# Performance work log

Measured on AMD Instinct MI355X. Metric: run time of the kernel, lower is better.

## Reference

```python
import jax, jax.numpy as jnp
import numpy as np

GROUP = 32          # microscale group size for both acts and weights
FP8_MAX = 448.0     # float8_e4m3fn max
FP4_TABLE = jnp.array([0.0, 0.5, 1.0, 1.5, 2.0, 3.0, 4.0, 6.0,
                       -0.0, -0.5, -1.0, -1.5, -2.0, -3.0, -4.0, -6.0], dtype=jnp.float32)


def _ue8m0_to_float(sf):
    # uint8 exponent byte placed directly into the fp32 exponent field: 2^(e-127)
    return jax.lax.bitcast_convert_type(sf.astype(jnp.uint32) << 23, jnp.float32)


def _dequant_mxfp4(w_packed, sf):
    # w_packed: [..., K//2] ints in [0,256), two e2m1 nibbles per byte (low nibble = even elem)
    lo = FP4_TABLE[w_packed & 0xF]
    hi = FP4_TABLE[(w_packed >> 4) & 0xF]
    w = jnp.stack([lo, hi], axis=-1).reshape(*w_packed.shape[:-1], -1)   # [..., K]
    s = _ue8m0_to_float(sf)                                              # [..., K//32]
    w = w.reshape(*sf.shape, GROUP) * s[..., None]
    return w.reshape(*w_packed.shape[:-1], 2 * w_packed.shape[-1])


def _quant_dequant_fp8(x):
    # Faithful to _deepseek_v4_stage_mega_moe_inputs_kernel: per-32-group amax,
    # scale = amax/448 rounded UP to a power of two (UE8M0), cast to fp8 e4m3.
    T, D = x.shape
    xg = x.reshape(T, D // GROUP, GROUP)
    amax = jnp.maximum(jnp.max(jnp.abs(xg), axis=-1), 1e-4)
    scale = amax / FP8_MAX
    bits = jax.lax.bitcast_convert_type(scale, jnp.uint32)
    exp = ((bits >> 23) & 0xFF) + ((bits & 0x7FFFFF) != 0).astype(jnp.uint32)
    exp = jnp.clip(exp, 1, 254)
    rscale = jax.lax.bitcast_convert_type(exp << 23, jnp.float32)
    q = (xg * (1.0 / rscale)[..., None]).astype(jnp.float8_e4m3fn)
    return (q.astype(jnp.float32) * rscale[..., None]).reshape(T, D)


def setup_inputs() -> dict:
    key = jax.random.key(0)
    ks = jax.random.split(key, 7)
    T, D, I, E, K = 512, 2048, 768, 16, 8
    hidden_states = jax.random.normal(ks[0], (T, D), dtype=jnp.float32)
    topk_weights = jax.random.uniform(ks[1], (T, K), dtype=jnp.float32)
    topk_weights = topk_weights / jnp.sum(topk_weights, axis=-1, keepdims=True)
    topk_ids = jax.random.randint(ks[2], (T, K), 0, E, dtype=jnp.int32)
    w13_weight = jax.random.randint(ks[3], (E, 2 * I, D // 2), 0, 256, dtype=jnp.int32)
    w13_weight_scale = jax.random.randint(ks[4], (E, 2 * I, D // GROUP), 120, 128, dtype=jnp.int32)
    w2_weight = jax.random.randint(ks[5], (E, D, I // 2), 0, 256, dtype=jnp.int32)
    w2_weight_scale = jax.random.randint(ks[6], (E, D, I // GROUP), 120, 128, dtype=jnp.int32)
    return {"hidden_states": hidden_states, "topk_weights": topk_weights,
            "topk_ids": topk_ids, "w13_weight": w13_weight,
            "w13_weight_scale": w13_weight_scale, "w2_weight": w2_weight,
            "w2_weight_scale": w2_weight_scale}


def reference(hidden_states, topk_weights, topk_ids, w13_weight, w13_weight_scale,
              w2_weight, w2_weight_scale):
    E = w13_weight.shape[0]
    I = w13_weight.shape[1] // 2
    x = _quant_dequant_fp8(hidden_states)                 # [T, D] fp8-quantized acts
    w13 = _dequant_mxfp4(w13_weight, w13_weight_scale)    # [E, 2I, D]
    w2 = _dequant_mxfp4(w2_weight, w2_weight_scale)       # [E, D, I]
    onehot = (topk_ids[:, :, None] == jnp.arange(E)[None, None, :]).astype(jnp.float32)  # [T,K,E]
    routed = jnp.any(onehot > 0, axis=1)                  # [T, E]
    Xe = routed.T[:, :, None].astype(x.dtype) * x[None]   # [E, T, D]
    h = jnp.einsum('etd,efd->etf', Xe, w13)               # [E, T, 2I]
    gate, up = h[..., :I], h[..., I:]
    a = jax.nn.silu(gate) * up                            # SiluAndMul
    ye = jnp.einsum('eti,edi->etd', a, w2)                # [E, T, D]
    comb = jnp.einsum('tke,tk->te', onehot, topk_weights) # [T, E] routing weights
    return jnp.einsum('te,etd->td', comb, ye)             # [T, D]
```

## Files before the change

### kernel.cpp

```cpp
#include <hip/hip_runtime.h>
#include <stdint.h>
#include <math.h>

#define T_TOK 512
#define DDIM  2048
#define IDIM  768
#define NEXP  16
#define TOPK  8
#define LDB   72

typedef __attribute__((ext_vector_type(8))) short bf16x8;
typedef __attribute__((ext_vector_type(4))) float f32x4;

__device__ __forceinline__ float e4m3_rtne(float f) {
  uint32_t u = __float_as_uint(f);
  uint32_t sign = u & 0x80000000u;
  uint32_t a = u & 0x7FFFFFFFu;
  float fa = __uint_as_float(a);
  float out;
  if (fa >= 0.015625f) {
    uint32_t lsb = (a >> 20) & 1u;
    a += 0x0007FFFFu + lsb;
    a &= 0xFFF00000u;
    out = __uint_as_float(a);
  } else {
    out = rintf(fa * 512.0f) * 0.001953125f;
  }
  return __uint_as_float(__float_as_uint(out) | sign);
}

__global__ void qdq_kernel(const float* __restrict__ x, ushort* __restrict__ xq) {
  int idx = blockIdx.x * 256 + threadIdx.x;
  float v = x[idx];
  float a = fabsf(v);
#pragma unroll
  for (int m = 16; m >= 1; m >>= 1)
    a = fmaxf(a, __shfl_xor(a, m, 32));
  a = fmaxf(a, 1e-4f);
  float scale = a / 448.0f;
  uint32_t b = __float_as_uint(scale);
  uint32_t ex = ((b >> 23) & 255u) + ((b & 0x7FFFFFu) ? 1u : 0u);
  ex = ex < 1u ? 1u : (ex > 254u ? 254u : ex);
  float rscale = __uint_as_float(ex << 23);
  float inv = 1.0f / rscale;
  float r = e4m3_rtne(v * inv) * rscale;
  xq[idx] = (ushort)(__float_as_uint(r) >> 16);
}

__global__ void route_kernel(const int* __restrict__ ids, const float* __restrict__ wts,
                             int* counts, int* offsets, int* lists, float* combs,
                             int* tpe, int* tps, int* tpn) {
  int t = threadIdx.x;
  int  myid[TOPK];
  float myw[TOPK];
#pragma unroll
  for (int k = 0; k < TOPK; k++) { myid[k] = ids[t*TOPK+k]; myw[k] = wts[t*TOPK+k]; }
  int np = 0;
  for (int e = 0; e < NEXP; e++) {
    float s = 0.f; bool r = false;
#pragma unroll
    for (int k = 0; k < TOPK; k++) if (myid[k] == e) { s += myw[k]; r = true; }
    if (r) {
      int slot = atomicAdd(&counts[e], 1);
      lists[(e<<9) + slot] = t;
      combs[(e<<9) + slot] = s;
      tpe[t*TOPK + np] = e;
      tps[t*TOPK + np] = slot;
      np++;
    }
  }
  tpn[t] = np;
  __syncthreads();
  if (t == 0) {
    int acc = 0;
    for (int e = 0; e < NEXP; e++) {
      offsets[e] = acc;
      acc += atomicAdd(&counts[e], 0);
    }
    offsets[NEXP] = acc;
  }
}

__device__ __forceinline__ uint32_t dec2(uint32_t w8, uint32_t S) {
  uint32_t lo = w8 & 15u, hi = (w8 >> 4) & 15u;
  uint32_t mlo = lo & 7u, mhi = hi & 7u;
  uint32_t clo = (mlo < 2u) ? 0u : mlo;
  uint32_t chi = (mhi < 2u) ? 0u : mhi;
  uint32_t blo = (mlo == 0u) ? 0u : ((S + clo) << 6);
  uint32_t bhi = (mhi == 0u) ? 0u : ((S + chi) << 6);
  blo |= (lo & 8u) << 12;
  bhi |= (hi & 8u) << 12;
  return blo | (bhi << 16);
}

__global__ __launch_bounds__(256,3) void gemm1_kernel(
    const ushort* __restrict__ xq, const int* __restrict__ w13,
    const int* __restrict__ w13s, const int* __restrict__ counts,
    const int* __restrict__ offsets, const int* __restrict__ lists,
    const float* __restrict__ combs, ushort* __restrict__ a_buf)
{
  const int e  = blockIdx.x;
  const int i0 = blockIdx.y << 5;
  const int m0 = blockIdx.z << 7;
  const int cnt = counts[e];
  if (m0 >= cnt) return;

  __shared__ __align__(16) ushort Bsh[2][64*LDB];
  __shared__ int   toks[128];
  __shared__ float cmbs[128];

  const int tid = threadIdx.x;
  if (tid < 128) {
    int m = m0 + tid; bool v = m < cnt;
    toks[tid] = v ? lists[(e<<9)+m] : 0;
    cmbs[tid] = v ? combs[(e<<9)+m] : 0.f;
  }
  __syncthreads();

  const int wv = tid >> 6, l = tid & 63, l16 = l & 15, q = l >> 4;

  const ushort* arow[2];
#pragma unroll
  for (int i = 0; i < 2; i++)
    arow[i] = xq + (size_t)toks[wv*32 + i*16 + l16]*DDIM + q*8;

  const int rb = tid >> 2, hq = tid & 3;
  const int feat = (rb < 32) ? (i0 + rb) : (IDIM + i0 + (rb - 32));
  const int* wrow = w13 + ((size_t)e*(2*IDIM) + feat)*(DDIM/2) + hq*8;
  const int* srow = w13s + ((size_t)e*(2*IDIM) + feat)*(DDIM/32) + (hq >> 1);
  const int bdst = rb*LDB + hq*16;

  f32x4 acc[2][4];
#pragma unroll
  for (int i = 0; i < 2; i++)
#pragma unroll
    for (int j = 0; j < 4; j++) acc[i][j] = (f32x4){0.f,0.f,0.f,0.f};

  bf16x8 afr[2][2];
#pragma unroll
  for (int i = 0; i < 2; i++)
#pragma unroll
    for (int s = 0; s < 2; s++)
      afr[i][s] = *(const bf16x8*)(arow[i] + s*32);
  {
    int4 w0 = *(const int4*)(wrow);
    int4 w1 = *(const int4*)(wrow + 4);
    uint32_t S = (((uint32_t)srow[0]) - 1u) << 1;
    int wi[8] = {w0.x,w0.y,w0.z,w0.w, w1.x,w1.y,w1.z,w1.w};
    uint32_t od[8];
#pragma unroll
    for (int c = 0; c < 8; c++) od[c] = dec2((uint32_t)wi[c], S);
    ushort* d = &Bsh[0][bdst];
    *(uint4*)d       = make_uint4(od[0], od[1], od[2], od[3]);
    *(uint4*)(d + 8) = make_uint4(od[4], od[5], od[6], od[7]);
  }
  __syncthreads();

  for (int k0 = 0; k0 < DDIM; k0 += 64) {
    const int cur = (k0 >> 6) & 1;
    const bool more = (k0 + 64) < DDIM;

    int4 nw0, nw1; uint32_t nS = 0;
    bf16x8 nafr[2][2];
    if (more) {
      const int* wp = wrow + ((k0 + 64) >> 1);
      nw0 = *(const int4*)wp;
      nw1 = *(const int4*)(wp + 4);
      nS = (((uint32_t)srow[(k0 + 64) >> 5]) - 1u) << 1;
#pragma unroll
      for (int i = 0; i < 2; i++)
#pragma unroll
        for (int s = 0; s < 2; s++)
          nafr[i][s] = *(const bf16x8*)(arow[i] + k0 + 64 + s*32);
    }

#pragma unroll
    for (int s = 0; s < 2; s++) {
      bf16x8 bfr[4];
#pragma unroll
      for (int j = 0; j < 4; j++)
        bfr[j] = *(const bf16x8*)&Bsh[cur][(j*16 + l16)*LDB + s*32 + q*8];
#pragma unroll
      for (int i = 0; i < 2; i++)
#pragma unroll
        for (int j = 0; j < 4; j++)
          acc[i][j] = __builtin_amdgcn_mfma_f32_16x16x32_bf16(afr[i][s], bfr[j], acc[i][j], 0, 0, 0);
    }

    if (more) {
      int wi[8] = {nw0.x,nw0.y,nw0.z,nw0.w, nw1.x,nw1.y,nw1.z,nw1.w};
      uint32_t od[8];
#pragma unroll
      for (int c = 0; c < 8; c++) od[c] = dec2((uint32_t)wi[c], nS);
      ushort* d = &Bsh[1 - cur][bdst];
      *(uint4*)d       = make_uint4(od[0], od[1], od[2], od[3]);
      *(uint4*)(d + 8) = make_uint4(od[4], od[5], od[6], od[7]);
#pragma unroll
      for (int i = 0; i < 2; i++)
#pragma unroll
        for (int s = 0; s < 2; s++)
          afr[i][s] = nafr[i][s];
    }
    __syncthreads();
  }

  const int obase = offsets[e];
#pragma unroll
  for (int i = 0; i < 2; i++) {
#pragma unroll
    for (int r = 0; r < 4; r++) {
      int mrow = wv*32 + i*16 + q*4 + r;
      int gm = m0 + mrow;
      if (gm < cnt) {
        float c = cmbs[mrow];
        ushort* dst = a_buf + (size_t)(obase + gm)*IDIM + i0 + l16;
#pragma unroll
        for (int jj = 0; jj < 2; jj++) {
          float g = acc[i][jj][r], u = acc[i][jj+2][r];
          float val = (g / (1.f + expf(-g))) * u * c;
          uint32_t bb = __float_as_uint(val);
          bb += 0x7FFFu + ((bb >> 16) & 1u);
          dst[jj*16] = (ushort)(bb >> 16);
        }
      }
    }
  }
}

__global__ __launch_bounds__(256,3) void gemm2_kernel(
    const ushort* __restrict__ a_buf, const int* __restrict__ w2,
    const int* __restrict__ w2s, const int* __restrict__ counts,
    const int* __restrict__ offsets, const int* __restrict__ lists,
    float* __restrict__ out, ushort* __restrict__ ye, int use_ye)
{
  const int e  = blockIdx.x;
  const int n0 = blockIdx.y << 6;
  const int m0 = blockIdx.z << 7;
  const int cnt = counts[e];
  if (m0 >= cnt) return;

  __shared__ __align__(16) ushort Bsh[2][64*LDB];
  __shared__ int toks[128];

  const int tid = threadIdx.x;
  if (tid < 128) {
    int m = m0 + tid;
    toks[tid] = (m < cnt) ? lists[(e<<9)+m] : -1;
  }
  __syncthreads();

  const int wv = tid >> 6, l = tid & 63, l16 = l & 15, q = l >> 4;
  const int obase = offsets[e];

  const ushort* arow[2];
#pragma unroll
  for (int i = 0; i < 2; i++) {
    int gm = m0 + wv*32 + i*16 + l16;
    int rowc = (gm < cnt) ? gm : 0;
    arow[i] = a_buf + (size_t)(obase + rowc)*IDIM + q*8;
  }

  const int rb = tid >> 2, hq = tid & 3;
  const int* wrow = w2 + ((size_t)e*DDIM + n0 + rb)*(IDIM/2) + hq*8;
  const int* srow = w2s + ((size_t)e*DDIM + n0 + rb)*(IDIM/32) + (hq >> 1);
  const int bdst = rb*LDB + hq*16;

  f32x4 acc[2][4];
#pragma unroll
  for (int i = 0; i < 2; i++)
#pragma unroll
    for (int j = 0; j < 4; j++) acc[i][j] = (f32x4){0.f,0.f,0.f,0.f};

  bf16x8 afr[2][2];
#pragma unroll
  for (int i = 0; i < 2; i++)
#pragma unroll
    for (int s = 0; s < 2; s++)
      afr[i][s] = *(const bf16x8*)(arow[i] + s*32);
  {
    int4 w0 = *(const int4*)(wrow);
    int4 w1 = *(const int4*)(wrow + 4);
    uint32_t S = (((uint32_t)srow[0]) - 1u) << 1;
    int wi[8] = {w0.x,w0.y,w0.z,w0.w, w1.x,w1.y,w1.z,w1.w};
    uint32_t od[8];
#pragma unroll
    for (int c = 0; c < 8; c++) od[c] = dec2((uint32_t)wi[c], S);
    ushort* d = &Bsh[0][bdst];
    *(uint4*)d       = make_uint4(od[0], od[1], od[2], od[3]);
    *(uint4*)(d + 8) = make_uint4(od[4], od[5], od[6], od[7]);
  }
  __syncthreads();

  for (int k0 = 0; k0 < IDIM; k0 += 64) {
    const int cur = (k0 >> 6) & 1;
    const bool more = (k0 + 64) < IDIM;

    int4 nw0, nw1; uint32_t nS = 0;
    bf16x8 nafr[2][2];
    if (more) {
      const int* wp = wrow + ((k0 + 64) >> 1);
      nw0 = *(const int4*)wp;
      nw1 = *(const int4*)(wp + 4);
      nS = (((uint32_t)srow[(k0 + 64) >> 5]) - 1u) << 1;
#pragma unroll
      for (int i = 0; i < 2; i++)
#pragma unroll
        for (int s = 0; s < 2; s++)
          nafr[i][s] = *(const bf16x8*)(arow[i] + k0 + 64 + s*32);
    }

#pragma unroll
    for (int s = 0; s < 2; s++) {
      bf16x8 bfr[4];
#pragma unroll
      for (int j = 0; j < 4; j++)
        bfr[j] = *(const bf16x8*)&Bsh[cur][(j*16 + l16)*LDB + s*32 + q*8];
#pragma unroll
      for (int i = 0; i < 2; i++)
#pragma unroll
        for (int j = 0; j < 4; j++)
          acc[i][j] = __builtin_amdgcn_mfma_f32_16x16x32_bf16(afr[i][s], bfr[j], acc[i][j], 0, 0, 0);
    }

    if (more) {
      int wi[8] = {nw0.x,nw0.y,nw0.z,nw0.w, nw1.x,nw1.y,nw1.z,nw1.w};
      uint32_t od[8];
#pragma unroll
      for (int c = 0; c < 8; c++) od[c] = dec2((uint32_t)wi[c], nS);
      ushort* d = &Bsh[1 - cur][bdst];
      *(uint4*)d       = make_uint4(od[0], od[1], od[2], od[3]);
      *(uint4*)(d + 8) = make_uint4(od[4], od[5], od[6], od[7]);
#pragma unroll
      for (int i = 0; i < 2; i++)
#pragma unroll
        for (int s = 0; s < 2; s++)
          afr[i][s] = nafr[i][s];
    }
    __syncthreads();
  }

#pragma unroll
  for (int i = 0; i < 2; i++) {
#pragma unroll
    for (int r = 0; r < 4; r++) {
      int mrow = wv*32 + i*16 + q*4 + r;
      int gm = m0 + mrow;
      if (gm < cnt) {
        if (use_ye) {
          ushort* dst = ye + (size_t)(obase + gm)*DDIM + n0 + l16;
#pragma unroll
          for (int j = 0; j < 4; j++) {
            uint32_t bb = __float_as_uint(acc[i][j][r]);
            bb += 0x7FFFu + ((bb >> 16) & 1u);
            dst[j*16] = (ushort)(bb >> 16);
          }
        } else {
          int tok = toks[mrow];
          float* dst = out + (size_t)tok*DDIM + n0 + l16;
#pragma unroll
          for (int j = 0; j < 4; j++) atomicAdd(&dst[j*16], acc[i][j][r]);
        }
      }
    }
  }
}

__global__ void combine_kernel(const ushort* __restrict__ ye, const int* __restrict__ offsets,
                               const int* __restrict__ tpe, const int* __restrict__ tps,
                               const int* __restrict__ tpn, float* __restrict__ out) {
  int t = blockIdx.x;
  int np = tpn[t];
  int rows[TOPK];
#pragma unroll
  for (int j = 0; j < TOPK; j++)
    rows[j] = (j < np) ? (offsets[tpe[t*TOPK+j]] + tps[t*TOPK+j]) : -1;
  for (int c = threadIdx.x; c < DDIM; c += 256) {
    float s = 0.f;
#pragma unroll
    for (int j = 0; j < TOPK; j++)
      if (rows[j] >= 0)
        s += __uint_as_float(((uint32_t)ye[(size_t)rows[j]*DDIM + c]) << 16);
    out[(size_t)t*DDIM + c] = s;
  }
}

extern "C" void kernel_launch(void* const* d_in, const int* in_sizes, int n_in,
                              void* d_out, int out_size, void* d_ws, size_t ws_size,
                              hipStream_t stream)
{
  const float* x    = (const float*)d_in[0];
  const float* tw   = (const float*)d_in[1];
  const int*   tids = (const int*)d_in[2];
  const int*   w13  = (const int*)d_in[3];
  const int*   w13s = (const int*)d_in[4];
  const int*   w2   = (const int*)d_in[5];
  const int*   w2s  = (const int*)d_in[6];
  float* out = (float*)d_out;

  char* ws = (char*)d_ws;
  size_t off = 0;
  auto alloc = [&](size_t bytes) { void* p = ws + off; off = (off + bytes + 255) & ~(size_t)255; return p; };
  ushort* xq     = (ushort*)alloc((size_t)T_TOK*DDIM*2);
  int*   counts  = (int*)alloc(64*4);
  int*   offsets = (int*)alloc(64*4);
  int*   lists   = (int*)alloc((size_t)NEXP*T_TOK*4);
  float* combs   = (float*)alloc((size_t)NEXP*T_TOK*4);
  int*   tpe     = (int*)alloc((size_t)T_TOK*TOPK*4);
  int*   tps     = (int*)alloc((size_t)T_TOK*TOPK*4);
  int*   tpn     = (int*)alloc((size_t)T_TOK*4);
  ushort* a_buf  = (ushort*)alloc((size_t)T_TOK*TOPK*IDIM*2);
  ushort* ye     = (ushort*)(ws + off);
  size_t need_ye = off + (size_t)T_TOK*TOPK*DDIM*2;
  int use_ye = (ws_size >= need_ye) ? 1 : 0;

  hipMemsetAsync(counts, 0, 256, stream);
  hipMemsetAsync(out, 0, (size_t)out_size * 4, stream);

  qdq_kernel<<<(T_TOK*DDIM)/256, 256, 0, stream>>>(x, xq);
  route_kernel<<<1, T_TOK, 0, stream>>>(tids, tw, counts, offsets, lists, combs, tpe, tps, tpn);
  gemm1_kernel<<<dim3(NEXP, IDIM/32, 4), 256, 0, stream>>>(
      xq, w13, w13s, counts, offsets, lists, combs, a_buf);
  gemm2_kernel<<<dim3(NEXP, DDIM/64, 4), 256, 0, stream>>>(
      a_buf, w2, w2s, counts, offsets, lists, out, ye, use_ye);
  if (use_ye)
    combine_kernel<<<T_TOK, 256, 0, stream>>>(ye, offsets, tpe, tps, tpn, out);
}
```

Measured before the change: 315.0 us.

## Split gemm2 and combine into column chunks with a smaller ye buffer

The second GEMM and the combine step now run in four passes over 512-column slices of the output dimension, so the intermediate ye buffer needs only a quarter of the workspace. This lets the deterministic non-atomic combine path fit in smaller workspaces and keeps each slice of ye more likely to stay cache-resident between the write and the read. Routing metadata is also packed into short lists and a single packed ushort per token-expert pair. The cost is extra kernel launches, and each gemm2 pass fills the GPU with fewer blocks.

```diff
diff --git a/kernel.cpp b/kernel.cpp
--- a/kernel.cpp
+++ b/kernel.cpp
@@ -8,6 +8,7 @@
 #define NEXP  16
 #define TOPK  8
 #define LDB   72
+#define YW    512
 
 typedef __attribute__((ext_vector_type(8))) short bf16x8;
 typedef __attribute__((ext_vector_type(4))) float f32x4;
@@ -48,8 +49,8 @@
 }
 
 __global__ void route_kernel(const int* __restrict__ ids, const float* __restrict__ wts,
-                             int* counts, int* offsets, int* lists, float* combs,
-                             int* tpe, int* tps, int* tpn) {
+                             int* counts, int* offsets, short* lists, float* combs,
+                             ushort* tpp, int* tpn) {
   int t = threadIdx.x;
   int  myid[TOPK];
   float myw[TOPK];
@@ -62,10 +63,9 @@
     for (int k = 0; k < TOPK; k++) if (myid[k] == e) { s += myw[k]; r = true; }
     if (r) {
       int slot = atomicAdd(&counts[e], 1);
-      lists[(e<<9) + slot] = t;
+      lists[(e<<9) + slot] = (short)t;
       combs[(e<<9) + slot] = s;
-      tpe[t*TOPK + np] = e;
-      tps[t*TOPK + np] = slot;
+      tpp[t*TOPK + np] = (ushort)((e << 12) | slot);
       np++;
     }
   }
@@ -96,7 +96,7 @@
 __global__ __launch_bounds__(256,3) void gemm1_kernel(
     const ushort* __restrict__ xq, const int* __restrict__ w13,
     const int* __restrict__ w13s, const int* __restrict__ counts,
-    const int* __restrict__ offsets, const int* __restrict__ lists,
+    const int* __restrict__ offsets, const short* __restrict__ lists,
     const float* __restrict__ combs, ushort* __restrict__ a_buf)
 {
   const int e  = blockIdx.x;
@@ -112,7 +112,7 @@
   const int tid = threadIdx.x;
   if (tid < 128) {
     int m = m0 + tid; bool v = m < cnt;
-    toks[tid] = v ? lists[(e<<9)+m] : 0;
+    toks[tid] = v ? (int)lists[(e<<9)+m] : 0;
     cmbs[tid] = v ? combs[(e<<9)+m] : 0.f;
   }
   __syncthreads();
@@ -230,11 +230,11 @@
 __global__ __launch_bounds__(256,3) void gemm2_kernel(
     const ushort* __restrict__ a_buf, const int* __restrict__ w2,
     const int* __restrict__ w2s, const int* __restrict__ counts,
-    const int* __restrict__ offsets, const int* __restrict__ lists,
-    float* __restrict__ out, ushort* __restrict__ ye, int use_ye)
+    const int* __restrict__ offsets, const short* __restrict__ lists,
+    float* __restrict__ out, ushort* __restrict__ ye, int use_ye, int yb)
 {
   const int e  = blockIdx.x;
-  const int n0 = blockIdx.y << 6;
+  const int n0 = yb + (blockIdx.y << 6);
   const int m0 = blockIdx.z << 7;
   const int cnt = counts[e];
   if (m0 >= cnt) return;
@@ -245,7 +245,7 @@
   const int tid = threadIdx.x;
   if (tid < 128) {
     int m = m0 + tid;
-    toks[tid] = (m < cnt) ? lists[(e<<9)+m] : -1;
+    toks[tid] = (m < cnt) ? (int)lists[(e<<9)+m] : -1;
   }
   __syncthreads();
 
@@ -347,7 +347,7 @@
       int gm = m0 + mrow;
       if (gm < cnt) {
         if (use_ye) {
-          ushort* dst = ye + (size_t)(obase + gm)*DDIM + n0 + l16;
+          ushort* dst = ye + (size_t)(obase + gm)*YW + (n0 - yb) + l16;
 #pragma unroll
           for (int j = 0; j < 4; j++) {
             uint32_t bb = __float_as_uint(acc[i][j][r]);
@@ -366,21 +366,25 @@
 }
 
 __global__ void combine_kernel(const ushort* __restrict__ ye, const int* __restrict__ offsets,
-                               const int* __restrict__ tpe, const int* __restrict__ tps,
-                               const int* __restrict__ tpn, float* __restrict__ out) {
+                               const ushort* __restrict__ tpp, const int* __restrict__ tpn,
+                               float* __restrict__ out, int yb) {
   int t = blockIdx.x;
   int np = tpn[t];
   int rows[TOPK];
 #pragma unroll
-  for (int j = 0; j < TOPK; j++)
-    rows[j] = (j < np) ? (offsets[tpe[t*TOPK+j]] + tps[t*TOPK+j]) : -1;
-  for (int c = threadIdx.x; c < DDIM; c += 256) {
+  for (int j = 0; j < TOPK; j++) {
+    if (j < np) {
+      uint32_t v = tpp[t*TOPK + j];
+      rows[j] = offsets[v >> 12] + (int)(v & 0xFFFu);
+    } else rows[j] = -1;
+  }
+  for (int c = threadIdx.x; c < YW; c += 256) {
     float s = 0.f;
 #pragma unroll
     for (int j = 0; j < TOPK; j++)
       if (rows[j] >= 0)
-        s += __uint_as_float(((uint32_t)ye[(size_t)rows[j]*DDIM + c]) << 16);
-    out[(size_t)t*DDIM + c] = s;
+        s += __uint_as_float(((uint32_t)ye[(size_t)rows[j]*YW + c]) << 16);
+    out[(size_t)t*DDIM + yb + c] = s;
   }
 }
 
@@ -400,28 +404,29 @@
   char* ws = (char*)d_ws;
   size_t off = 0;
   auto alloc = [&](size_t bytes) { void* p = ws + off; off = (off + bytes + 255) & ~(size_t)255; return p; };
+  ushort* a_buf  = (ushort*)alloc((size_t)T_TOK*TOPK*IDIM*2);
+  ushort* ye     = (ushort*)alloc((size_t)T_TOK*TOPK*YW*2);
   ushort* xq     = (ushort*)alloc((size_t)T_TOK*DDIM*2);
+  float* combs   = (float*)alloc((size_t)NEXP*T_TOK*4);
+  short* lists   = (short*)alloc((size_t)NEXP*T_TOK*2);
+  ushort* tpp    = (ushort*)alloc((size_t)T_TOK*TOPK*2);
+  int*   tpn     = (int*)alloc((size_t)T_TOK*4);
   int*   counts  = (int*)alloc(64*4);
   int*   offsets = (int*)alloc(64*4);
-  int*   lists   = (int*)alloc((size_t)NEXP*T_TOK*4);
-  float* combs   = (float*)alloc((size_t)NEXP*T_TOK*4);
-  int*   tpe     = (int*)alloc((size_t)T_TOK*TOPK*4);
-  int*   tps     = (int*)alloc((size_t)T_TOK*TOPK*4);
-  int*   tpn     = (int*)alloc((size_t)T_TOK*4);
-  ushort* a_buf  = (ushort*)alloc((size_t)T_TOK*TOPK*IDIM*2);
-  ushort* ye     = (ushort*)(ws + off);
-  size_t need_ye = off + (size_t)T_TOK*TOPK*DDIM*2;
-  int use_ye = (ws_size >= need_ye) ? 1 : 0;
+  size_t need = off;
+  int use_ye = (ws_size >= need) ? 1 : 0;
 
   hipMemsetAsync(counts, 0, 256, stream);
   hipMemsetAsync(out, 0, (size_t)out_size * 4, stream);
 
   qdq_kernel<<<(T_TOK*DDIM)/256, 256, 0, stream>>>(x, xq);
-  route_kernel<<<1, T_TOK, 0, stream>>>(tids, tw, counts, offsets, lists, combs, tpe, tps, tpn);
+  route_kernel<<<1, T_TOK, 0, stream>>>(tids, tw, counts, offsets, lists, combs, tpp, tpn);
   gemm1_kernel<<<dim3(NEXP, IDIM/32, 4), 256, 0, stream>>>(
       xq, w13, w13s, counts, offsets, lists, combs, a_buf);
-  gemm2_kernel<<<dim3(NEXP, DDIM/64, 4), 256, 0, stream>>>(
-      a_buf, w2, w2s, counts, offsets, lists, out, ye, use_ye);
-  if (use_ye)
-    combine_kernel<<<T_TOK, 256, 0, stream>>>(ye, offsets, tpe, tps, tpn, out);
-}
+  for (int p = 0; p < DDIM/YW; p++) {
+    gemm2_kernel<<<dim3(NEXP, YW/64, 4), 256, 0, stream>>>(
+        a_buf, w2, w2s, counts, offsets, lists, out, ye, use_ye, p*YW);
+    if (use_ye)
+      combine_kernel<<<T_TOK, 256, 0, stream>>>(ye, offsets, tpp, tpn, out, p*YW);
+  }
+}
```

Result: slower. 369.8 us (+17.4%).
